# Kernel optimization log

Measured on AMD Instinct MI355X. Metric: run time of the kernel, lower is better.

## Reference

```python
import jax, jax.numpy as jnp
import numpy as np

HEADS = 8
DIM_HEAD = 64
DIM = HEADS * DIM_HEAD  # 512
EPS = 1e-5


def setup_inputs() -> dict:
    key = jax.random.key(0)
    k1, k2, k3 = jax.random.split(key, 3)
    B, D, H, W, C = 2, 8, 64, 64, 256
    x = jax.random.normal(k1, (B, D, H, W, C), dtype=jnp.float32)
    # 1x1x1 convs are pointwise linear maps
    w_qkv = jax.random.normal(k2, (C, 3 * DIM), dtype=jnp.float32) * (1.0 / np.sqrt(C))
    w_out = jax.random.normal(k3, (DIM, C), dtype=jnp.float32) * (1.0 / np.sqrt(DIM))
    b_out = jnp.zeros((C,), dtype=jnp.float32)
    ln_scale = jnp.ones((C,), dtype=jnp.float32)
    return {"x": x, "w_qkv": w_qkv, "w_out": w_out, "b_out": b_out, "ln_scale": ln_scale}


def reference(x, w_qkv, w_out, b_out, ln_scale):
    B, D, H, W, C = x.shape
    N = D * H * W
    # qkv projection (1x1x1 conv, no bias)
    qkv = jnp.einsum('bdhwc,cf->bdhwf', x, w_qkv)  # (B,D,H,W,3*DIM)
    q, k, v = jnp.split(qkv, 3, axis=-1)
    # 'b d h w (h d) -> b (d h w) h d' : heads-major channel split
    def to_tokens(t):
        return t.reshape(B, N, HEADS, DIM_HEAD)
    q, k, v = to_tokens(q), to_tokens(k), to_tokens(v)
    q = jax.nn.softmax(q, axis=-1) / jnp.sqrt(jnp.float32(DIM_HEAD))
    k = jax.nn.softmax(k, axis=1)   # softmax over token axis (axis=-3)
    v = v / jnp.float32(N)
    # context: K^T V per head, (B,HEADS,DIM_HEAD,DIM_HEAD)
    context = jnp.einsum('bnhd,bnhe->bhde', k, v)
    # out: Q @ context -> (B,N,HEADS,DIM_HEAD)
    out = jnp.einsum('bhde,bnhd->bnhe', context, q)
    out = out.reshape(B, D, H, W, DIM)
    # output projection (1x1x1 conv with bias)
    out = jnp.einsum('bdhwf,fc->bdhwc', out, w_out) + b_out
    # LayerNorm (scale only, no bias)
    mu = jnp.mean(out, axis=-1, keepdims=True)
    var = jnp.var(out, axis=-1, keepdims=True)
    out = (out - mu) * jax.lax.rsqrt(var + EPS) * ln_scale
    return out
```

## Files before the change

kernel.cpp:

```cpp
#include <hip/hip_runtime.h>
#include <cstdint>
#include <cstddef>

#define HEADS 8
#define DH 64
#define DIM 512
#define CIN 256
#define EPS 1e-5f
#define NB 64
#define BATCH 2
#define NTOK 32768

#define XPAD 264
#define TP 40

#define ZERO_FLOATS (BATCH * HEADS * DH * DH + BATCH * HEADS * DH)
#define ZERO_F4     (ZERO_FLOATS / 4)

typedef __attribute__((ext_vector_type(8))) short bf16x8;
typedef __attribute__((ext_vector_type(4))) float f32x4;

static __device__ __forceinline__ f32x4 mfma16(bf16x8 a, bf16x8 b, f32x4 c) {
  return __builtin_amdgcn_mfma_f32_16x16x32_bf16(a, b, c, 0, 0, 0);
}
static __device__ __forceinline__ unsigned short f2bf(float f) {
  unsigned int u = __float_as_uint(f);
  u += 0x7FFFu + ((u >> 16) & 1u);
  return (unsigned short)(u >> 16);
}
static __device__ __forceinline__ float bf2f(unsigned short h) {
  return __uint_as_float(((unsigned int)h) << 16);
}
static __device__ __forceinline__ void split2(float f, unsigned short& hi, unsigned short& lo) {
  hi = f2bf(f);
  lo = f2bf(f - bf2f(hi));
}

__global__ __launch_bounds__(256) void prep_wT(
    const float* __restrict__ wqkv, unsigned short* __restrict__ wThi,
    unsigned short* __restrict__ wTlo, float* __restrict__ zero_base)
{
  __shared__ __align__(16) unsigned short thi[64][68];
  __shared__ __align__(16) unsigned short tlo[64][68];
  const int tid = threadIdx.x;
  const int f0 = (blockIdx.x >> 2) * 64;
  const int k0 = (blockIdx.x & 3) * 64;

  {
    const int gid = blockIdx.x * 256 + tid;
    if (gid < ZERO_F4)
      ((float4*)zero_base)[gid] = make_float4(0.f, 0.f, 0.f, 0.f);
  }

  {
    const int kl = tid >> 2;
    const int fc = (tid & 3) * 16;
#pragma unroll
    for (int i = 0; i < 4; ++i) {
      const float4 v = *(const float4*)(wqkv + (size_t)(k0 + kl) * (3 * DIM) + f0 + fc + i * 4);
      unsigned short h, l;
      split2(v.x, h, l); thi[kl][fc + i*4 + 0] = h; tlo[kl][fc + i*4 + 0] = l;
      split2(v.y, h, l); thi[kl][fc + i*4 + 1] = h; tlo[kl][fc + i*4 + 1] = l;
      split2(v.z, h, l); thi[kl][fc + i*4 + 2] = h; tlo[kl][fc + i*4 + 2] = l;
      split2(v.w, h, l); thi[kl][fc + i*4 + 3] = h; tlo[kl][fc + i*4 + 3] = l;
    }
  }
  __syncthreads();
  {
    const int fl = tid >> 2;
    const int kc = (tid & 3) * 16;
    unsigned int ph[8], pl[8];
#pragma unroll
    for (int m = 0; m < 8; ++m) {
      ph[m] = (unsigned)thi[kc + 2*m][fl] | ((unsigned)thi[kc + 2*m + 1][fl] << 16);
      pl[m] = (unsigned)tlo[kc + 2*m][fl] | ((unsigned)tlo[kc + 2*m + 1][fl] << 16);
    }
    unsigned int* dh = (unsigned int*)(wThi + (size_t)(f0 + fl) * CIN + k0 + kc);
    unsigned int* dl = (unsigned int*)(wTlo + (size_t)(f0 + fl) * CIN + k0 + kc);
#pragma unroll
    for (int m = 0; m < 8; ++m) { dh[m] = ph[m]; dl[m] = pl[m]; }
  }
}

__global__ __launch_bounds__(256, 2) void kv_ctx_mfma(
    const float* __restrict__ x,
    const unsigned short* __restrict__ wThi, const unsigned short* __restrict__ wTlo,
    float* __restrict__ ctx_un, float* __restrict__ Ssum)
{
  __shared__ __align__(16) unsigned short xhi[32 * XPAD];
  __shared__ __align__(16) unsigned short xlo[32 * XPAD];
  __shared__ __align__(16) unsigned short ekhi[64 * TP];
  __shared__ __align__(16) unsigned short eklo[64 * TP];
  __shared__ __align__(16) unsigned short vhs[64 * TP];
  __shared__ __align__(16) unsigned short vls[64 * TP];

  const int tid = threadIdx.x;
  const int L = blockIdx.x;
  const int tb = (((L >> 6) & 7) << 3) | (L & 7);
  const int h  = (L >> 3) & 7;
  const int b  = L >> 9;
  const int n0 = tb * (NTOK / NB);

  const int wave = tid >> 6;
  const int lane = tid & 63;
  const int lg = lane >> 4;
  const int lr = lane & 15;

  const bool isv = wave >= 2;
  const int cbase = (wave & 1) * 32;
  const int wrow_base = (isv ? 2 * DIM : DIM) + h * DH + cbase;
  const unsigned short* whB = wThi + (size_t)wrow_base * CIN;
  const unsigned short* wlB = wTlo + (size_t)wrow_base * CIN;

  const short one_bf = (short)0x3F80;
  const bf16x8 bones = {one_bf, one_bf, one_bf, one_bf, one_bf, one_bf, one_bf, one_bf};

  f32x4 ctx[4];
#pragma unroll
  for (int et = 0; et < 4; ++et) ctx[et] = (f32x4)0.f;
  f32x4 acc_s = (f32x4)0.f;

  const int srow = tid >> 3;
  const int c0f  = (tid & 7) * 32;
  const float4* xg0 = (const float4*)(x + ((size_t)b * NTOK + n0) * CIN);

  float4 pf[8];
#pragma unroll
  for (int i = 0; i < 8; ++i) pf[i] = xg0[srow * 64 + (c0f >> 2) + i];

#pragma unroll 1
  for (int sub = 0; sub < 16; ++sub) {
    {
      unsigned short* dh = xhi + srow * XPAD + c0f;
      unsigned short* dl = xlo + srow * XPAD + c0f;
#pragma unroll
      for (int i = 0; i < 8; ++i) {
        const float4 v = pf[i];
        unsigned short h0,l0,h1,l1,h2,l2,h3,l3;
        split2(v.x,h0,l0); split2(v.y,h1,l1); split2(v.z,h2,l2); split2(v.w,h3,l3);
        *(uint2*)(dh + i*4) = make_uint2((unsigned)h0 | ((unsigned)h1 << 16),
                                         (unsigned)h2 | ((unsigned)h3 << 16));
        *(uint2*)(dl + i*4) = make_uint2((unsigned)l0 | ((unsigned)l1 << 16),
                                         (unsigned)l2 | ((unsigned)l3 << 16));
      }
    }
    if (sub + 1 < 16) {
      const float4* xg = xg0 + (size_t)(sub + 1) * 32 * 64;
#pragma unroll
      for (int i = 0; i < 8; ++i) pf[i] = xg[srow * 64 + (c0f >> 2) + i];
    }
    __syncthreads();

    f32x4 acc[2][2];
#pragma unroll
    for (int rt = 0; rt < 2; ++rt)
#pragma unroll
      for (int ct = 0; ct < 2; ++ct) acc[rt][ct] = (f32x4)0.f;

#pragma unroll
    for (int kk = 0; kk < 8; ++kk) {
      const bf16x8 a0h = *(const bf16x8*)(xhi + (0 + lr) * XPAD + kk * 32 + lg * 8);
      const bf16x8 a1h = *(const bf16x8*)(xhi + (16 + lr) * XPAD + kk * 32 + lg * 8);
      const bf16x8 a0l = *(const bf16x8*)(xlo + (0 + lr) * XPAD + kk * 32 + lg * 8);
      const bf16x8 a1l = *(const bf16x8*)(xlo + (16 + lr) * XPAD + kk * 32 + lg * 8);
#pragma unroll
      for (int ct = 0; ct < 2; ++ct) {
        const int rofs = (ct * 16 + lr) * CIN + kk * 32 + lg * 8;
        const bf16x8 bwh = *(const bf16x8*)(whB + rofs);
        const bf16x8 bwl = *(const bf16x8*)(wlB + rofs);
        acc[0][ct] = mfma16(a0h, bwh, acc[0][ct]);
        acc[0][ct] = mfma16(a0h, bwl, acc[0][ct]);
        acc[0][ct] = mfma16(a0l, bwh, acc[0][ct]);
        acc[1][ct] = mfma16(a1h, bwh, acc[1][ct]);
        acc[1][ct] = mfma16(a1h, bwl, acc[1][ct]);
        acc[1][ct] = mfma16(a1l, bwh, acc[1][ct]);
      }
    }

#pragma unroll
    for (int rt = 0; rt < 2; ++rt)
#pragma unroll
      for (int ct = 0; ct < 2; ++ct) {
        unsigned short hh[4], ll[4];
#pragma unroll
        for (int r = 0; r < 4; ++r) {
          float f = acc[rt][ct][r];
          if (!isv) f = __expf(f);
          split2(f, hh[r], ll[r]);
        }
        const int c = cbase + ct * 16 + lr;
        const int t0 = rt * 16 + lg * 4;
        unsigned short* ph = (isv ? vhs : ekhi) + c * TP + t0;
        unsigned short* pl = (isv ? vls : eklo) + c * TP + t0;
        *(uint2*)ph = make_uint2((unsigned)hh[0] | ((unsigned)hh[1] << 16),
                                 (unsigned)hh[2] | ((unsigned)hh[3] << 16));
        *(uint2*)pl = make_uint2((unsigned)ll[0] | ((unsigned)ll[1] << 16),
                                 (unsigned)ll[2] | ((unsigned)ll[3] << 16));
      }
    __syncthreads();

    {
      const int drow = wave * 16 + lr;
      const bf16x8 aeh = *(const bf16x8*)(ekhi + drow * TP + lg * 8);
      const bf16x8 ael = *(const bf16x8*)(eklo + drow * TP + lg * 8);
      acc_s = mfma16(aeh, bones, acc_s);
      acc_s = mfma16(ael, bones, acc_s);
#pragma unroll
      for (int et = 0; et < 4; ++et) {
        const bf16x8 bvh = *(const bf16x8*)(vhs + (et * 16 + lr) * TP + lg * 8);
        const bf16x8 bvl = *(const bf16x8*)(vls + (et * 16 + lr) * TP + lg * 8);
        ctx[et] = mfma16(aeh, bvh, ctx[et]);
        ctx[et] = mfma16(aeh, bvl, ctx[et]);
        ctx[et] = mfma16(ael, bvh, ctx[et]);
      }
    }
  }

  float* ctxb = ctx_un + ((size_t)b * HEADS + h) * DH * DH;
#pragma unroll
  for (int et = 0; et < 4; ++et)
#pragma unroll
    for (int r = 0; r < 4; ++r)
      atomicAdd(&ctxb[(wave * 16 + lg * 4 + r) * DH + et * 16 + lr], ctx[et][r]);
  if (lr == 0) {
#pragma unroll
    for (int r = 0; r < 4; ++r)
      atomicAdd(&Ssum[((size_t)b * HEADS + h) * DH + wave * 16 + lg * 4 + r], acc_s[r]);
  }
}

__global__ __launch_bounds__(256) void m_kernel(
    const float* __restrict__ ctx_un, const float* __restrict__ Ssum,
    const float* __restrict__ wout, unsigned short* __restrict__ MThi,
    unsigned short* __restrict__ MTlo, float invN)
{
  const int blk = blockIdx.x;
  const int b = blk >> 5;
  const int f0 = (blk & 31) * 16;
  const int h = f0 / DH;
  const int c = threadIdx.x;
  const float* ctxb = ctx_un + ((size_t)b * HEADS + h) * DH * DH;
  const float* Sb   = Ssum + ((size_t)b * HEADS + h) * DH;
  float acc[16];
#pragma unroll
  for (int i = 0; i < 16; ++i) acc[i] = 0.f;
  for (int e = 0; e < DH; ++e) {
    const float wv = wout[(size_t)(h * DH + e) * CIN + c];
#pragma unroll
    for (int i = 0; i < 16; ++i) {
      const int d = (f0 + i) & (DH - 1);
      acc[i] += ctxb[d * DH + e] * wv;
    }
  }
  unsigned short* mh = MThi + ((size_t)b * CIN + c) * DIM;
  unsigned short* ml = MTlo + ((size_t)b * CIN + c) * DIM;
#pragma unroll
  for (int i = 0; i < 16; ++i) {
    const int d = (f0 + i) & (DH - 1);
    unsigned short hh, ll;
    split2(acc[i] * (invN / Sb[d]), hh, ll);
    mh[f0 + i] = hh;
    ml[f0 + i] = ll;
  }
}

__global__ __launch_bounds__(256, 4) void out_mfma(
    const float* __restrict__ x,
    const unsigned short* __restrict__ wThi, const unsigned short* __restrict__ wTlo,
    const unsigned short* __restrict__ MThi, const unsigned short* __restrict__ MTlo,
    const float* __restrict__ bout, const float* __restrict__ lnsc,
    float* __restrict__ out)
{
  __shared__ __align__(16) unsigned short ldsA[2 * 32 * XPAD];
  __shared__ float red[4][32][2];
  __shared__ float mus[32], rss[32];

  unsigned short* const xh = ldsA;
  unsigned short* const xl = ldsA + 32 * XPAD;
  unsigned short* const qh = ldsA;
  unsigned short* const ql = ldsA + 32 * XPAD;

  const int tid = threadIdx.x;
  const int blk = blockIdx.x;
  const int blocks_per_b = NTOK / 32;
  const int b = blk / blocks_per_b;
  const int n0 = (blk % blocks_per_b) * 32;

  const int wave = tid >> 6;
  const int lane = tid & 63;
  const int lg = lane >> 4;
  const int lr = lane & 15;

  {
    const int row = tid >> 3;
    const int c0f = (tid & 7) * 32;
    const float4* xg = (const float4*)(x + ((size_t)b * NTOK + n0) * CIN);
    unsigned short* dh = xh + row * XPAD + c0f;
    unsigned short* dl = xl + row * XPAD + c0f;
#pragma unroll
    for (int i = 0; i < 8; ++i) {
      const float4 v = xg[row * 64 + (c0f >> 2) + i];
      unsigned short h0,l0,h1,l1,h2,l2,h3,l3;
      split2(v.x,h0,l0); split2(v.y,h1,l1); split2(v.z,h2,l2); split2(v.w,h3,l3);
      *(uint2*)(dh + i*4) = make_uint2((unsigned)h0 | ((unsigned)h1 << 16),
                                       (unsigned)h2 | ((unsigned)h3 << 16));
      *(uint2*)(dl + i*4) = make_uint2((unsigned)l0 | ((unsigned)l1 << 16),
                                       (unsigned)l2 | ((unsigned)l3 << 16));
    }
  }
  __syncthreads();

  f32x4 q[2][8];
#pragma unroll
  for (int rt = 0; rt < 2; ++rt)
#pragma unroll
    for (int ct = 0; ct < 8; ++ct) q[rt][ct] = (f32x4)0.f;

#pragma unroll 2
  for (int kk = 0; kk < 8; ++kk) {
    const bf16x8 a0h = *(const bf16x8*)(xh + (0 + lr) * XPAD + kk * 32 + lg * 8);
    const bf16x8 a1h = *(const bf16x8*)(xh + (16 + lr) * XPAD + kk * 32 + lg * 8);
    const bf16x8 a0l = *(const bf16x8*)(xl + (0 + lr) * XPAD + kk * 32 + lg * 8);
    const bf16x8 a1l = *(const bf16x8*)(xl + (16 + lr) * XPAD + kk * 32 + lg * 8);
#pragma unroll
    for (int ct = 0; ct < 8; ++ct) {
      const size_t row = (size_t)(wave * 128 + ct * 16 + lr);
      const bf16x8 bwh = *(const bf16x8*)(wThi + row * CIN + kk * 32 + lg * 8);
      const bf16x8 bwl = *(const bf16x8*)(wTlo + row * CIN + kk * 32 + lg * 8);
      q[0][ct] = mfma16(a0h, bwh, q[0][ct]);
      q[0][ct] = mfma16(a0h, bwl, q[0][ct]);
      q[0][ct] = mfma16(a0l, bwh, q[0][ct]);
      q[1][ct] = mfma16(a1h, bwh, q[1][ct]);
      q[1][ct] = mfma16(a1h, bwl, q[1][ct]);
      q[1][ct] = mfma16(a1l, bwh, q[1][ct]);
    }
  }

#pragma unroll
  for (int rt = 0; rt < 2; ++rt)
#pragma unroll
    for (int hg = 0; hg < 2; ++hg)
#pragma unroll
      for (int r = 0; r < 4; ++r) {
        float m0 = fmaxf(fmaxf(q[rt][hg*4+0][r], q[rt][hg*4+1][r]),
                         fmaxf(q[rt][hg*4+2][r], q[rt][hg*4+3][r]));
#pragma unroll
        for (int off = 1; off < 16; off <<= 1)
          m0 = fmaxf(m0, __shfl_xor(m0, off, 16));
        const float e0v = __expf(q[rt][hg*4+0][r] - m0);
        const float e1v = __expf(q[rt][hg*4+1][r] - m0);
        const float e2v = __expf(q[rt][hg*4+2][r] - m0);
        const float e3v = __expf(q[rt][hg*4+3][r] - m0);
        float s = e0v + e1v + e2v + e3v;
#pragma unroll
        for (int off = 1; off < 16; off <<= 1)
          s += __shfl_xor(s, off, 16);
        const float sc = 0.125f / s;
        q[rt][hg*4+0][r] = e0v * sc;
        q[rt][hg*4+1][r] = e1v * sc;
        q[rt][hg*4+2][r] = e2v * sc;
        q[rt][hg*4+3][r] = e3v * sc;
      }

  __syncthreads();

  if (wave < 2) {
#pragma unroll
    for (int rt = 0; rt < 2; ++rt)
#pragma unroll
      for (int ct = 0; ct < 8; ++ct)
#pragma unroll
        for (int r = 0; r < 4; ++r) {
          const int t = rt * 16 + lg * 4 + r;
          const int col = wave * 128 + ct * 16 + lr;
          unsigned short hh, ll;
          split2(q[rt][ct][r], hh, ll);
          qh[t * XPAD + col] = hh;
          ql[t * XPAD + col] = ll;
        }
  }
  __syncthreads();

  f32x4 y[2][4];
#pragma unroll
  for (int rt = 0; rt < 2; ++rt)
#pragma unroll
    for (int ct = 0; ct < 4; ++ct) y[rt][ct] = (f32x4)0.f;

  const unsigned short* mhB = MThi + (size_t)b * CIN * DIM;
  const unsigned short* mlB = MTlo + (size_t)b * CIN * DIM;

#pragma unroll
  for (int pass = 0; pass < 2; ++pass) {
    const int fofs = pass * 256;
#pragma unroll 2
    for (int kk = 0; kk < 8; ++kk) {
      const bf16x8 a0h = *(const bf16x8*)(qh + (0 + lr) * XPAD + kk * 32 + lg * 8);
      const bf16x8 a1h = *(const bf16x8*)(qh + (16 + lr) * XPAD + kk * 32 + lg * 8);
      const bf16x8 a0l = *(const bf16x8*)(ql + (0 + lr) * XPAD + kk * 32 + lg * 8);
      const bf16x8 a1l = *(const bf16x8*)(ql + (16 + lr) * XPAD + kk * 32 + lg * 8);
#pragma unroll
      for (int ct = 0; ct < 4; ++ct) {
        const size_t crow = (size_t)(wave * 64 + ct * 16 + lr);
        const bf16x8 bmh = *(const bf16x8*)(mhB + crow * DIM + fofs + kk * 32 + lg * 8);
        const bf16x8 bml = *(const bf16x8*)(mlB + crow * DIM + fofs + kk * 32 + lg * 8);
        y[0][ct] = mfma16(a0h, bmh, y[0][ct]);
        y[0][ct] = mfma16(a0h, bml, y[0][ct]);
        y[0][ct] = mfma16(a0l, bmh, y[0][ct]);
        y[1][ct] = mfma16(a1h, bmh, y[1][ct]);
        y[1][ct] = mfma16(a1h, bml, y[1][ct]);
        y[1][ct] = mfma16(a1l, bmh, y[1][ct]);
      }
    }
    if (pass == 0) {
      __syncthreads();
      if (wave >= 2) {
#pragma unroll
        for (int rt = 0; rt < 2; ++rt)
#pragma unroll
          for (int ct = 0; ct < 8; ++ct)
#pragma unroll
            for (int r = 0; r < 4; ++r) {
              const int t = rt * 16 + lg * 4 + r;
              const int col = wave * 128 + ct * 16 + lr - 256;
              unsigned short hh, ll;
              split2(q[rt][ct][r], hh, ll);
              qh[t * XPAD + col] = hh;
              ql[t * XPAD + col] = ll;
            }
      }
      __syncthreads();
    }
  }

#pragma unroll
  for (int ct = 0; ct < 4; ++ct) {
    const float bb = bout[wave * 64 + ct * 16 + lr];
#pragma unroll
    for (int rt = 0; rt < 2; ++rt)
#pragma unroll
      for (int r = 0; r < 4; ++r) y[rt][ct][r] += bb;
  }

#pragma unroll
  for (int rt = 0; rt < 2; ++rt)
#pragma unroll
    for (int r = 0; r < 4; ++r) {
      float ps = y[rt][0][r] + y[rt][1][r] + y[rt][2][r] + y[rt][3][r];
      float ps2 = y[rt][0][r]*y[rt][0][r] + y[rt][1][r]*y[rt][1][r]
                + y[rt][2][r]*y[rt][2][r] + y[rt][3][r]*y[rt][3][r];
#pragma unroll
      for (int off = 1; off < 16; off <<= 1) {
        ps  += __shfl_xor(ps,  off, 16);
        ps2 += __shfl_xor(ps2, off, 16);
      }
      if (lr == 0) {
        const int t = rt * 16 + lg * 4 + r;
        red[wave][t][0] = ps;
        red[wave][t][1] = ps2;
      }
    }
  __syncthreads();
  if (tid < 32) {
    const float S1 = red[0][tid][0] + red[1][tid][0] + red[2][tid][0] + red[3][tid][0];
    const float S2 = red[0][tid][1] + red[1][tid][1] + red[2][tid][1] + red[3][tid][1];
    const float mu = S1 * (1.f / CIN);
    const float var = S2 * (1.f / CIN) - mu * mu;
    mus[tid] = mu;
    rss[tid] = rsqrtf(var + EPS);
  }
  __syncthreads();

  float* ob = out + ((size_t)b * NTOK + n0) * CIN;
#pragma unroll
  for (int ct = 0; ct < 4; ++ct) {
    const int c = wave * 64 + ct * 16 + lr;
    const float lsc = lnsc[c];
#pragma unroll
    for (int rt = 0; rt < 2; ++rt)
#pragma unroll
      for (int r = 0; r < 4; ++r) {
        const int t = rt * 16 + lg * 4 + r;
        ob[(size_t)t * CIN + c] = (y[rt][ct][r] - mus[t]) * rss[t] * lsc;
      }
  }
}

extern "C" void kernel_launch(void* const* d_in, const int* in_sizes, int n_in,
                              void* d_out, int out_size, void* d_ws, size_t ws_size,
                              hipStream_t stream) {
  const float* x     = (const float*)d_in[0];
  const float* wqkv  = (const float*)d_in[1];
  const float* wout  = (const float*)d_in[2];
  const float* bout  = (const float*)d_in[3];
  const float* lnsc  = (const float*)d_in[4];
  float* out = (float*)d_out;

  unsigned short* wThi = (unsigned short*)d_ws;
  unsigned short* wTlo = wThi + (size_t)(3 * DIM) * CIN;
  unsigned short* MThi = wTlo + (size_t)(3 * DIM) * CIN;
  unsigned short* MTlo = MThi + (size_t)BATCH * CIN * DIM;
  float* ctx_un = (float*)(MTlo + (size_t)BATCH * CIN * DIM);
  float* Ssum   = ctx_un + (size_t)BATCH * HEADS * DH * DH;

  prep_wT<<<dim3(96), dim3(256), 0, stream>>>(wqkv, wThi, wTlo, ctx_un);
  kv_ctx_mfma<<<dim3(BATCH * HEADS * NB), dim3(256), 0, stream>>>(
      x, wThi, wTlo, ctx_un, Ssum);
  m_kernel<<<dim3(BATCH * 32), dim3(256), 0, stream>>>(
      ctx_un, Ssum, wout, MThi, MTlo, 1.0f / (float)NTOK);
  out_mfma<<<dim3(BATCH * (NTOK / 32)), dim3(256), 0, stream>>>(
      x, wThi, wTlo, MThi, MTlo, bout, lnsc, out);
}
```

Before: 556.2 us.

## Pre-split x to bf16 hi/lo once and widen output kernel to 512 threads

Adds a split_x kernel that converts x into bf16 hi/lo planes once in workspace (when the workspace is large enough), so kv_ctx_mfma and out_mfma load pre-split bf16 instead of re-splitting fp32 per block. out_mfma moves to 512 threads with 8 waves, each owning one head for the q-softmax, stores the full 512-wide q tile in LDS with an XOR swizzle instead of two passes, and reduces LayerNorm partials across 8 waves. kv_ctx raises the occupancy hint and shrinks the LDS padding, loading via 8-byte pieces. The cost is an extra full pass writing and reading a 64MB split copy of x plus higher LDS use per block.

```diff
diff --git a/kernel.cpp b/kernel.cpp
--- a/kernel.cpp
+++ b/kernel.cpp
@@ -12,10 +12,9 @@
 #define NTOK 32768
 
 #define XPAD 264
-#define TP 40
-
-#define ZERO_FLOATS (BATCH * HEADS * DH * DH + BATCH * HEADS * DH)
-#define ZERO_F4     (ZERO_FLOATS / 4)
+#define TP 36
+
+#define ZERO_F4 16640
 
 typedef __attribute__((ext_vector_type(8))) short bf16x8;
 typedef __attribute__((ext_vector_type(4))) float f32x4;
@@ -34,6 +33,33 @@
 static __device__ __forceinline__ void split2(float f, unsigned short& hi, unsigned short& lo) {
   hi = f2bf(f);
   lo = f2bf(f - bf2f(hi));
+}
+static __device__ __forceinline__ bf16x8 ld_b8(const unsigned short* p) {
+  union { bf16x8 v; uint2 u[2]; } t;
+  t.u[0] = *(const uint2*)p;
+  t.u[1] = *(const uint2*)(p + 4);
+  return t.v;
+}
+
+__global__ __launch_bounds__(256) void split_x(
+    const float* __restrict__ x, unsigned short* __restrict__ xh,
+    unsigned short* __restrict__ xl)
+{
+  const float4* xf = (const float4*)x;
+  uint2* oh = (uint2*)xh;
+  uint2* ol = (uint2*)xl;
+  const int base = blockIdx.x * 256 + threadIdx.x;
+#pragma unroll
+  for (int j = 0; j < 4; ++j) {
+    const size_t p = (size_t)base + (size_t)j * 1048576;
+    const float4 v = xf[p];
+    unsigned short h0,l0,h1,l1,h2,l2,h3,l3;
+    split2(v.x,h0,l0); split2(v.y,h1,l1); split2(v.z,h2,l2); split2(v.w,h3,l3);
+    oh[p] = make_uint2((unsigned)h0 | ((unsigned)h1 << 16),
+                       (unsigned)h2 | ((unsigned)h3 << 16));
+    ol[p] = make_uint2((unsigned)l0 | ((unsigned)l1 << 16),
+                       (unsigned)l2 | ((unsigned)l3 << 16));
+  }
 }
 
 __global__ __launch_bounds__(256) void prep_wT(
@@ -51,7 +77,6 @@
     if (gid < ZERO_F4)
       ((float4*)zero_base)[gid] = make_float4(0.f, 0.f, 0.f, 0.f);
   }
-
   {
     const int kl = tid >> 2;
     const int fc = (tid & 3) * 16;
@@ -82,8 +107,10 @@
   }
 }
 
-__global__ __launch_bounds__(256, 2) void kv_ctx_mfma(
+template<bool PRESPLIT>
+__global__ __launch_bounds__(256, 3) void kv_ctx_mfma(
     const float* __restrict__ x,
+    const unsigned short* __restrict__ xhg, const unsigned short* __restrict__ xlg,
     const unsigned short* __restrict__ wThi, const unsigned short* __restrict__ wTlo,
     float* __restrict__ ctx_un, float* __restrict__ Ssum)
 {
@@ -121,18 +148,36 @@
   f32x4 acc_s = (f32x4)0.f;
 
   const int srow = tid >> 3;
-  const int c0f  = (tid & 7) * 32;
-  const float4* xg0 = (const float4*)(x + ((size_t)b * NTOK + n0) * CIN);
-
+  const int cch  = tid & 7;
+
+  uint4 ph[4], pl[4];
   float4 pf[8];
-#pragma unroll
-  for (int i = 0; i < 8; ++i) pf[i] = xg0[srow * 64 + (c0f >> 2) + i];
+
+  if constexpr (PRESPLIT) {
+    const uint4* gh = (const uint4*)(xhg + ((size_t)b * NTOK + n0) * CIN);
+    const uint4* gl = (const uint4*)(xlg + ((size_t)b * NTOK + n0) * CIN);
+#pragma unroll
+    for (int i = 0; i < 4; ++i) {
+      ph[i] = gh[srow * 32 + cch + i * 8];
+      pl[i] = gl[srow * 32 + cch + i * 8];
+    }
+  } else {
+    const float4* xg0 = (const float4*)(x + ((size_t)b * NTOK + n0) * CIN);
+#pragma unroll
+    for (int i = 0; i < 8; ++i) pf[i] = xg0[srow * 64 + cch * 8 + i];
+  }
 
 #pragma unroll 1
   for (int sub = 0; sub < 16; ++sub) {
-    {
-      unsigned short* dh = xhi + srow * XPAD + c0f;
-      unsigned short* dl = xlo + srow * XPAD + c0f;
+    if constexpr (PRESPLIT) {
+#pragma unroll
+      for (int i = 0; i < 4; ++i) {
+        *(uint4*)(xhi + srow * XPAD + (cch + i * 8) * 8) = ph[i];
+        *(uint4*)(xlo + srow * XPAD + (cch + i * 8) * 8) = pl[i];
+      }
+    } else {
+      unsigned short* dh = xhi + srow * XPAD + cch * 32;
+      unsigned short* dl = xlo + srow * XPAD + cch * 32;
 #pragma unroll
       for (int i = 0; i < 8; ++i) {
         const float4 v = pf[i];
@@ -145,9 +190,20 @@
       }
     }
     if (sub + 1 < 16) {
-      const float4* xg = xg0 + (size_t)(sub + 1) * 32 * 64;
-#pragma unroll
-      for (int i = 0; i < 8; ++i) pf[i] = xg[srow * 64 + (c0f >> 2) + i];
+      const int nn = n0 + (sub + 1) * 32;
+      if constexpr (PRESPLIT) {
+        const uint4* gh = (const uint4*)(xhg + ((size_t)b * NTOK + nn) * CIN);
+        const uint4* gl = (const uint4*)(xlg + ((size_t)b * NTOK + nn) * CIN);
+#pragma unroll
+        for (int i = 0; i < 4; ++i) {
+          ph[i] = gh[srow * 32 + cch + i * 8];
+          pl[i] = gl[srow * 32 + cch + i * 8];
+        }
+      } else {
+        const float4* xg = (const float4*)(x + ((size_t)b * NTOK + nn) * CIN);
+#pragma unroll
+        for (int i = 0; i < 8; ++i) pf[i] = xg[srow * 64 + cch * 8 + i];
+      }
     }
     __syncthreads();
 
@@ -190,25 +246,25 @@
         }
         const int c = cbase + ct * 16 + lr;
         const int t0 = rt * 16 + lg * 4;
-        unsigned short* ph = (isv ? vhs : ekhi) + c * TP + t0;
-        unsigned short* pl = (isv ? vls : eklo) + c * TP + t0;
-        *(uint2*)ph = make_uint2((unsigned)hh[0] | ((unsigned)hh[1] << 16),
-                                 (unsigned)hh[2] | ((unsigned)hh[3] << 16));
-        *(uint2*)pl = make_uint2((unsigned)ll[0] | ((unsigned)ll[1] << 16),
-                                 (unsigned)ll[2] | ((unsigned)ll[3] << 16));
+        unsigned short* phd = (isv ? vhs : ekhi) + c * TP + t0;
+        unsigned short* pld = (isv ? vls : eklo) + c * TP + t0;
+        *(uint2*)phd = make_uint2((unsigned)hh[0] | ((unsigned)hh[1] << 16),
+                                  (unsigned)hh[2] | ((unsigned)hh[3] << 16));
+        *(uint2*)pld = make_uint2((unsigned)ll[0] | ((unsigned)ll[1] << 16),
+                                  (unsigned)ll[2] | ((unsigned)ll[3] << 16));
       }
     __syncthreads();
 
     {
       const int drow = wave * 16 + lr;
-      const bf16x8 aeh = *(const bf16x8*)(ekhi + drow * TP + lg * 8);
-      const bf16x8 ael = *(const bf16x8*)(eklo + drow * TP + lg * 8);
+      const bf16x8 aeh = ld_b8(ekhi + drow * TP + lg * 8);
+      const bf16x8 ael = ld_b8(eklo + drow * TP + lg * 8);
       acc_s = mfma16(aeh, bones, acc_s);
       acc_s = mfma16(ael, bones, acc_s);
 #pragma unroll
       for (int et = 0; et < 4; ++et) {
-        const bf16x8 bvh = *(const bf16x8*)(vhs + (et * 16 + lr) * TP + lg * 8);
-        const bf16x8 bvl = *(const bf16x8*)(vls + (et * 16 + lr) * TP + lg * 8);
+        const bf16x8 bvh = ld_b8(vhs + (et * 16 + lr) * TP + lg * 8);
+        const bf16x8 bvl = ld_b8(vls + (et * 16 + lr) * TP + lg * 8);
         ctx[et] = mfma16(aeh, bvh, ctx[et]);
         ctx[et] = mfma16(aeh, bvl, ctx[et]);
         ctx[et] = mfma16(ael, bvh, ctx[et]);
@@ -264,27 +320,27 @@
   }
 }
 
-__global__ __launch_bounds__(256, 4) void out_mfma(
+template<bool PRESPLIT>
+__global__ __launch_bounds__(512, 4) void out_mfma(
     const float* __restrict__ x,
+    const unsigned short* __restrict__ xhg, const unsigned short* __restrict__ xlg,
     const unsigned short* __restrict__ wThi, const unsigned short* __restrict__ wTlo,
     const unsigned short* __restrict__ MThi, const unsigned short* __restrict__ MTlo,
     const float* __restrict__ bout, const float* __restrict__ lnsc,
     float* __restrict__ out)
 {
-  __shared__ __align__(16) unsigned short ldsA[2 * 32 * XPAD];
-  __shared__ float red[4][32][2];
-  __shared__ float mus[32], rss[32];
-
-  unsigned short* const xh = ldsA;
-  unsigned short* const xl = ldsA + 32 * XPAD;
-  unsigned short* const qh = ldsA;
-  unsigned short* const ql = ldsA + 32 * XPAD;
+  __shared__ __align__(16) unsigned short buf[32768];
+
+  unsigned short* const xh  = buf;
+  unsigned short* const xl  = buf + 32 * XPAD;
+  unsigned short* const qhi = buf;
+  unsigned short* const qlo = buf + 32 * 512;
+  float* const redf = (float*)buf;
 
   const int tid = threadIdx.x;
   const int blk = blockIdx.x;
-  const int blocks_per_b = NTOK / 32;
-  const int b = blk / blocks_per_b;
-  const int n0 = (blk % blocks_per_b) * 32;
+  const int b = blk / (NTOK / 32);
+  const int n0 = (blk % (NTOK / 32)) * 32;
 
   const int wave = tid >> 6;
   const int lane = tid & 63;
@@ -292,29 +348,39 @@
   const int lr = lane & 15;
 
   {
-    const int row = tid >> 3;
-    const int c0f = (tid & 7) * 32;
-    const float4* xg = (const float4*)(x + ((size_t)b * NTOK + n0) * CIN);
-    unsigned short* dh = xh + row * XPAD + c0f;
-    unsigned short* dl = xl + row * XPAD + c0f;
-#pragma unroll
-    for (int i = 0; i < 8; ++i) {
-      const float4 v = xg[row * 64 + (c0f >> 2) + i];
-      unsigned short h0,l0,h1,l1,h2,l2,h3,l3;
-      split2(v.x,h0,l0); split2(v.y,h1,l1); split2(v.z,h2,l2); split2(v.w,h3,l3);
-      *(uint2*)(dh + i*4) = make_uint2((unsigned)h0 | ((unsigned)h1 << 16),
-                                       (unsigned)h2 | ((unsigned)h3 << 16));
-      *(uint2*)(dl + i*4) = make_uint2((unsigned)l0 | ((unsigned)l1 << 16),
-                                       (unsigned)l2 | ((unsigned)l3 << 16));
-    }
-  }
-  __syncthreads();
-
-  f32x4 q[2][8];
+    const int row = tid >> 4;
+    const int cu  = tid & 15;
+    if constexpr (PRESPLIT) {
+      const uint4* gh = (const uint4*)(xhg + ((size_t)b * NTOK + n0) * CIN);
+      const uint4* gl = (const uint4*)(xlg + ((size_t)b * NTOK + n0) * CIN);
+#pragma unroll
+      for (int i = 0; i < 2; ++i) {
+        const int u = cu + i * 16;
+        *(uint4*)(xh + row * XPAD + u * 8) = gh[row * 32 + u];
+        *(uint4*)(xl + row * XPAD + u * 8) = gl[row * 32 + u];
+      }
+    } else {
+      const float4* xg = (const float4*)(x + ((size_t)b * NTOK + n0) * CIN);
+#pragma unroll
+      for (int i = 0; i < 4; ++i) {
+        const int u = cu + i * 16;
+        const float4 v = xg[row * 64 + u];
+        unsigned short h0,l0,h1,l1,h2,l2,h3,l3;
+        split2(v.x,h0,l0); split2(v.y,h1,l1); split2(v.z,h2,l2); split2(v.w,h3,l3);
+        *(uint2*)(xh + row*XPAD + u*4) = make_uint2((unsigned)h0 | ((unsigned)h1 << 16),
+                                                    (unsigned)h2 | ((unsigned)h3 << 16));
+        *(uint2*)(xl + row*XPAD + u*4) = make_uint2((unsigned)l0 | ((unsigned)l1 << 16),
+                                                    (unsigned)l2 | ((unsigned)l3 << 16));
+      }
+    }
+  }
+  __syncthreads();
+
+  f32x4 q[2][4];
 #pragma unroll
   for (int rt = 0; rt < 2; ++rt)
 #pragma unroll
-    for (int ct = 0; ct < 8; ++ct) q[rt][ct] = (f32x4)0.f;
+    for (int ct = 0; ct < 4; ++ct) q[rt][ct] = (f32x4)0.f;
 
 #pragma unroll 2
   for (int kk = 0; kk < 8; ++kk) {
@@ -323,8 +389,8 @@
     const bf16x8 a0l = *(const bf16x8*)(xl + (0 + lr) * XPAD + kk * 32 + lg * 8);
     const bf16x8 a1l = *(const bf16x8*)(xl + (16 + lr) * XPAD + kk * 32 + lg * 8);
 #pragma unroll
-    for (int ct = 0; ct < 8; ++ct) {
-      const size_t row = (size_t)(wave * 128 + ct * 16 + lr);
+    for (int ct = 0; ct < 4; ++ct) {
+      const size_t row = (size_t)(wave * 64 + ct * 16 + lr);
       const bf16x8 bwh = *(const bf16x8*)(wThi + row * CIN + kk * 32 + lg * 8);
       const bf16x8 bwl = *(const bf16x8*)(wTlo + row * CIN + kk * 32 + lg * 8);
       q[0][ct] = mfma16(a0h, bwh, q[0][ct]);
@@ -339,116 +405,92 @@
 #pragma unroll
   for (int rt = 0; rt < 2; ++rt)
 #pragma unroll
-    for (int hg = 0; hg < 2; ++hg)
+    for (int r = 0; r < 4; ++r) {
+      float m0 = fmaxf(fmaxf(q[rt][0][r], q[rt][1][r]),
+                       fmaxf(q[rt][2][r], q[rt][3][r]));
+#pragma unroll
+      for (int off = 1; off < 16; off <<= 1)
+        m0 = fmaxf(m0, __shfl_xor(m0, off, 16));
+      const float e0v = __expf(q[rt][0][r] - m0);
+      const float e1v = __expf(q[rt][1][r] - m0);
+      const float e2v = __expf(q[rt][2][r] - m0);
+      const float e3v = __expf(q[rt][3][r] - m0);
+      float s = e0v + e1v + e2v + e3v;
+#pragma unroll
+      for (int off = 1; off < 16; off <<= 1)
+        s += __shfl_xor(s, off, 16);
+      const float sc = 0.125f / s;
+      q[rt][0][r] = e0v * sc;
+      q[rt][1][r] = e1v * sc;
+      q[rt][2][r] = e2v * sc;
+      q[rt][3][r] = e3v * sc;
+    }
+
+  __syncthreads();
+
+#pragma unroll
+  for (int rt = 0; rt < 2; ++rt)
+#pragma unroll
+    for (int ct = 0; ct < 4; ++ct)
 #pragma unroll
       for (int r = 0; r < 4; ++r) {
-        float m0 = fmaxf(fmaxf(q[rt][hg*4+0][r], q[rt][hg*4+1][r]),
-                         fmaxf(q[rt][hg*4+2][r], q[rt][hg*4+3][r]));
-#pragma unroll
-        for (int off = 1; off < 16; off <<= 1)
-          m0 = fmaxf(m0, __shfl_xor(m0, off, 16));
-        const float e0v = __expf(q[rt][hg*4+0][r] - m0);
-        const float e1v = __expf(q[rt][hg*4+1][r] - m0);
-        const float e2v = __expf(q[rt][hg*4+2][r] - m0);
-        const float e3v = __expf(q[rt][hg*4+3][r] - m0);
-        float s = e0v + e1v + e2v + e3v;
-#pragma unroll
-        for (int off = 1; off < 16; off <<= 1)
-          s += __shfl_xor(s, off, 16);
-        const float sc = 0.125f / s;
-        q[rt][hg*4+0][r] = e0v * sc;
-        q[rt][hg*4+1][r] = e1v * sc;
-        q[rt][hg*4+2][r] = e2v * sc;
-        q[rt][hg*4+3][r] = e3v * sc;
-      }
-
-  __syncthreads();
-
-  if (wave < 2) {
-#pragma unroll
-    for (int rt = 0; rt < 2; ++rt)
-#pragma unroll
-      for (int ct = 0; ct < 8; ++ct)
-#pragma unroll
-        for (int r = 0; r < 4; ++r) {
-          const int t = rt * 16 + lg * 4 + r;
-          const int col = wave * 128 + ct * 16 + lr;
-          unsigned short hh, ll;
-          split2(q[rt][ct][r], hh, ll);
-          qh[t * XPAD + col] = hh;
-          ql[t * XPAD + col] = ll;
-        }
-  }
-  __syncthreads();
-
-  f32x4 y[2][4];
+        const int t = rt * 16 + lg * 4 + r;
+        const int col = wave * 64 + ct * 16 + lr;
+        unsigned short hh, ll;
+        split2(q[rt][ct][r], hh, ll);
+        const int pos = t * 512 + ((((col >> 3) ^ (t & 15)) << 3) | (col & 7));
+        qhi[pos] = hh;
+        qlo[pos] = ll;
+      }
+  __syncthreads();
+
+  f32x4 y[2][2];
 #pragma unroll
   for (int rt = 0; rt < 2; ++rt)
 #pragma unroll
-    for (int ct = 0; ct < 4; ++ct) y[rt][ct] = (f32x4)0.f;
+    for (int ct = 0; ct < 2; ++ct) y[rt][ct] = (f32x4)0.f;
 
   const unsigned short* mhB = MThi + (size_t)b * CIN * DIM;
   const unsigned short* mlB = MTlo + (size_t)b * CIN * DIM;
 
-#pragma unroll
-  for (int pass = 0; pass < 2; ++pass) {
-    const int fofs = pass * 256;
 #pragma unroll 2
-    for (int kk = 0; kk < 8; ++kk) {
-      const bf16x8 a0h = *(const bf16x8*)(qh + (0 + lr) * XPAD + kk * 32 + lg * 8);
-      const bf16x8 a1h = *(const bf16x8*)(qh + (16 + lr) * XPAD + kk * 32 + lg * 8);
-      const bf16x8 a0l = *(const bf16x8*)(ql + (0 + lr) * XPAD + kk * 32 + lg * 8);
-      const bf16x8 a1l = *(const bf16x8*)(ql + (16 + lr) * XPAD + kk * 32 + lg * 8);
-#pragma unroll
-      for (int ct = 0; ct < 4; ++ct) {
-        const size_t crow = (size_t)(wave * 64 + ct * 16 + lr);
-        const bf16x8 bmh = *(const bf16x8*)(mhB + crow * DIM + fofs + kk * 32 + lg * 8);
-        const bf16x8 bml = *(const bf16x8*)(mlB + crow * DIM + fofs + kk * 32 + lg * 8);
-        y[0][ct] = mfma16(a0h, bmh, y[0][ct]);
-        y[0][ct] = mfma16(a0h, bml, y[0][ct]);
-        y[0][ct] = mfma16(a0l, bmh, y[0][ct]);
-        y[1][ct] = mfma16(a1h, bmh, y[1][ct]);
-        y[1][ct] = mfma16(a1h, bml, y[1][ct]);
-        y[1][ct] = mfma16(a1l, bmh, y[1][ct]);
-      }
-    }
-    if (pass == 0) {
-      __syncthreads();
-      if (wave >= 2) {
-#pragma unroll
-        for (int rt = 0; rt < 2; ++rt)
-#pragma unroll
-          for (int ct = 0; ct < 8; ++ct)
-#pragma unroll
-            for (int r = 0; r < 4; ++r) {
-              const int t = rt * 16 + lg * 4 + r;
-              const int col = wave * 128 + ct * 16 + lr - 256;
-              unsigned short hh, ll;
-              split2(q[rt][ct][r], hh, ll);
-              qh[t * XPAD + col] = hh;
-              ql[t * XPAD + col] = ll;
-            }
-      }
-      __syncthreads();
-    }
-  }
-
-#pragma unroll
-  for (int ct = 0; ct < 4; ++ct) {
-    const float bb = bout[wave * 64 + ct * 16 + lr];
+  for (int kk = 0; kk < 16; ++kk) {
+    const int sw = (((kk * 4 + lg) ^ lr) << 3);
+    const bf16x8 a0h = *(const bf16x8*)(qhi + (0 + lr) * 512 + sw);
+    const bf16x8 a1h = *(const bf16x8*)(qhi + (16 + lr) * 512 + sw);
+    const bf16x8 a0l = *(const bf16x8*)(qlo + (0 + lr) * 512 + sw);
+    const bf16x8 a1l = *(const bf16x8*)(qlo + (16 + lr) * 512 + sw);
+#pragma unroll
+    for (int ct = 0; ct < 2; ++ct) {
+      const size_t crow = (size_t)(wave * 32 + ct * 16 + lr);
+      const bf16x8 bmh = *(const bf16x8*)(mhB + crow * DIM + kk * 32 + lg * 8);
+      const bf16x8 bml = *(const bf16x8*)(mlB + crow * DIM + kk * 32 + lg * 8);
+      y[0][ct] = mfma16(a0h, bmh, y[0][ct]);
+      y[0][ct] = mfma16(a0h, bml, y[0][ct]);
+      y[0][ct] = mfma16(a0l, bmh, y[0][ct]);
+      y[1][ct] = mfma16(a1h, bmh, y[1][ct]);
+      y[1][ct] = mfma16(a1h, bml, y[1][ct]);
+      y[1][ct] = mfma16(a1l, bmh, y[1][ct]);
+    }
+  }
+
+#pragma unroll
+  for (int ct = 0; ct < 2; ++ct) {
+    const float bb = bout[wave * 32 + ct * 16 + lr];
 #pragma unroll
     for (int rt = 0; rt < 2; ++rt)
 #pragma unroll
       for (int r = 0; r < 4; ++r) y[rt][ct][r] += bb;
   }
 
+  __syncthreads();
+
 #pragma unroll
   for (int rt = 0; rt < 2; ++rt)
 #pragma unroll
     for (int r = 0; r < 4; ++r) {
-      float ps = y[rt][0][r] + y[rt][1][r] + y[rt][2][r] + y[rt][3][r];
-      float ps2 = y[rt][0][r]*y[rt][0][r] + y[rt][1][r]*y[rt][1][r]
-                + y[rt][2][r]*y[rt][2][r] + y[rt][3][r]*y[rt][3][r];
+      float ps = y[rt][0][r] + y[rt][1][r];
+      float ps2 = y[rt][0][r]*y[rt][0][r] + y[rt][1][r]*y[rt][1][r];
 #pragma unroll
       for (int off = 1; off < 16; off <<= 1) {
         ps  += __shfl_xor(ps,  off, 16);
@@ -456,32 +498,36 @@
       }
       if (lr == 0) {
         const int t = rt * 16 + lg * 4 + r;
-        red[wave][t][0] = ps;
-        red[wave][t][1] = ps2;
+        redf[(wave * 32 + t) * 2 + 0] = ps;
+        redf[(wave * 32 + t) * 2 + 1] = ps2;
       }
     }
   __syncthreads();
   if (tid < 32) {
-    const float S1 = red[0][tid][0] + red[1][tid][0] + red[2][tid][0] + red[3][tid][0];
-    const float S2 = red[0][tid][1] + red[1][tid][1] + red[2][tid][1] + red[3][tid][1];
+    float S1 = 0.f, S2 = 0.f;
+#pragma unroll
+    for (int w = 0; w < 8; ++w) {
+      S1 += redf[(w * 32 + tid) * 2 + 0];
+      S2 += redf[(w * 32 + tid) * 2 + 1];
+    }
     const float mu = S1 * (1.f / CIN);
     const float var = S2 * (1.f / CIN) - mu * mu;
-    mus[tid] = mu;
-    rss[tid] = rsqrtf(var + EPS);
+    redf[512 + tid] = mu;
+    redf[544 + tid] = rsqrtf(var + EPS);
   }
   __syncthreads();
 
   float* ob = out + ((size_t)b * NTOK + n0) * CIN;
 #pragma unroll
-  for (int ct = 0; ct < 4; ++ct) {
-    const int c = wave * 64 + ct * 16 + lr;
+  for (int ct = 0; ct < 2; ++ct) {
+    const int c = wave * 32 + ct * 16 + lr;
     const float lsc = lnsc[c];
 #pragma unroll
     for (int rt = 0; rt < 2; ++rt)
 #pragma unroll
       for (int r = 0; r < 4; ++r) {
         const int t = rt * 16 + lg * 4 + r;
-        ob[(size_t)t * CIN + c] = (y[rt][ct][r] - mus[t]) * rss[t] * lsc;
+        ob[(size_t)t * CIN + c] = (y[rt][ct][r] - redf[512 + t]) * redf[544 + t] * lsc;
       }
   }
 }
@@ -496,18 +542,33 @@
   const float* lnsc  = (const float*)d_in[4];
   float* out = (float*)d_out;
 
-  unsigned short* wThi = (unsigned short*)d_ws;
-  unsigned short* wTlo = wThi + (size_t)(3 * DIM) * CIN;
-  unsigned short* MThi = wTlo + (size_t)(3 * DIM) * CIN;
-  unsigned short* MTlo = MThi + (size_t)BATCH * CIN * DIM;
-  float* ctx_un = (float*)(MTlo + (size_t)BATCH * CIN * DIM);
-  float* Ssum   = ctx_un + (size_t)BATCH * HEADS * DH * DH;
+  unsigned char* w = (unsigned char*)d_ws;
+  unsigned short* wThi = (unsigned short*)(w + 0);
+  unsigned short* wTlo = (unsigned short*)(w + 786432);
+  unsigned short* MThi = (unsigned short*)(w + 1572864);
+  unsigned short* MTlo = (unsigned short*)(w + 2097152);
+  float* ctx_un = (float*)(w + 2621440);
+  float* Ssum   = (float*)(w + 2883584);
+  unsigned short* xhg = (unsigned short*)(w + 2887680);
+  unsigned short* xlg = (unsigned short*)(w + 2887680 + 33554432);
+  const bool presplit = ws_size >= (size_t)2887680 + 2u * 33554432u;
 
   prep_wT<<<dim3(96), dim3(256), 0, stream>>>(wqkv, wThi, wTlo, ctx_un);
-  kv_ctx_mfma<<<dim3(BATCH * HEADS * NB), dim3(256), 0, stream>>>(
-      x, wThi, wTlo, ctx_un, Ssum);
+  if (presplit) {
+    split_x<<<dim3(4096), dim3(256), 0, stream>>>(x, xhg, xlg);
+    kv_ctx_mfma<true><<<dim3(BATCH * HEADS * NB), dim3(256), 0, stream>>>(
+        x, xhg, xlg, wThi, wTlo, ctx_un, Ssum);
+  } else {
+    kv_ctx_mfma<false><<<dim3(BATCH * HEADS * NB), dim3(256), 0, stream>>>(
+        x, xhg, xlg, wThi, wTlo, ctx_un, Ssum);
+  }
   m_kernel<<<dim3(BATCH * 32), dim3(256), 0, stream>>>(
       ctx_un, Ssum, wout, MThi, MTlo, 1.0f / (float)NTOK);
-  out_mfma<<<dim3(BATCH * (NTOK / 32)), dim3(256), 0, stream>>>(
-      x, wThi, wTlo, MThi, MTlo, bout, lnsc, out);
-}
+  if (presplit) {
+    out_mfma<true><<<dim3(BATCH * (NTOK / 32)), dim3(512), 0, stream>>>(
+        x, xhg, xlg, wThi, wTlo, MThi, MTlo, bout, lnsc, out);
+  } else {
+    out_mfma<false><<<dim3(BATCH * (NTOK / 32)), dim3(512), 0, stream>>>(
+        x, xhg, xlg, wThi, wTlo, MThi, MTlo, bout, lnsc, out);
+  }
+}
```

Result: slower. 758.9 us (+36.4%).
